# Optimization experiments

Measured on AMD Instinct MI355X. Metric: run time of the kernel, lower is better.

## Reference

```python
import jax, jax.numpy as jnp
import numpy as np

N_NODES = 50000
N_EDGES = 600000
N_GRAPHS = 512
LN_EPS = 1e-5


def setup_inputs() -> dict:
    key = jax.random.key(0)
    ks = jax.random.split(key, 18)
    s = 0.05
    return {
        "x": jax.random.normal(ks[0], (N_NODES, 29), jnp.float32),
        "xdims": jax.random.normal(ks[1], (N_NODES, 3), jnp.float32),
        "xsttype": jax.random.randint(ks[2], (N_NODES,), 0, 256),
        "edge_index": jax.random.randint(ks[3], (2, N_EDGES), 0, N_NODES),
        "batch": jnp.sort(jax.random.randint(ks[4], (N_NODES,), 0, N_GRAPHS)),
        "st_emb": jax.random.normal(ks[5], (256, 12), jnp.float32) * s,
        "Wl1": jax.random.normal(ks[6], (128, 44), jnp.float32) * s,
        "bl1": jnp.zeros((128,), jnp.float32),
        "Wr1": jax.random.normal(ks[7], (128, 44), jnp.float32) * s,
        "g1": jnp.ones((128,), jnp.float32),
        "beta1": jnp.zeros((128,), jnp.float32),
        "Wl2": jax.random.normal(ks[8], (128, 128), jnp.float32) * s,
        "bl2": jnp.zeros((128,), jnp.float32),
        "Wr2": jax.random.normal(ks[9], (128, 128), jnp.float32) * s,
        "g2": jnp.ones((128,), jnp.float32),
        "beta2": jnp.zeros((128,), jnp.float32),
        "Wlin": jax.random.normal(ks[10], (10, 256), jnp.float32) * s,
        "blin": jnp.zeros((10,), jnp.float32),
    }


def layernorm(h, g, b):
    mu = jnp.mean(h, axis=-1, keepdims=True)
    var = jnp.mean(jnp.square(h - mu), axis=-1, keepdims=True)
    return g * (h - mu) * jax.lax.rsqrt(var + LN_EPS) + b


def sage_conv(h, src, dst, Wl, bl, Wr):
    # PyG SAGEConv: lin_l(mean_j x_j) + lin_r(x_i); messages flow src -> dst.
    msg = h[src]                                            # [E, D]
    agg = jax.ops.segment_sum(msg, dst, num_segments=N_NODES)
    cnt = jax.ops.segment_sum(jnp.ones((msg.shape[0],), h.dtype), dst, num_segments=N_NODES)
    mean = agg / jnp.maximum(cnt, 1.0)[:, None]
    return mean @ Wl.T + bl + h @ Wr.T


def reference(x, xdims, xsttype, edge_index, batch, st_emb,
              Wl1, bl1, Wr1, g1, beta1,
              Wl2, bl2, Wr2, g2, beta2,
              Wlin, blin):
    src, dst = edge_index[0], edge_index[1]
    h = jnp.concatenate([x, xdims, st_emb[xsttype]], axis=1)   # [N, 44]
    # Layer 1
    h = jax.nn.relu(layernorm(sage_conv(h, src, dst, Wl1, bl1, Wr1), g1, beta1))
    # Layer 2
    h = jax.nn.relu(layernorm(sage_conv(h, src, dst, Wl2, bl2, Wr2), g2, beta2))
    # dropout inactive (inference)
    hs = jax.ops.segment_sum(h, batch, num_segments=N_GRAPHS)
    nc = jax.ops.segment_sum(jnp.ones((h.shape[0],), h.dtype), batch, num_segments=N_GRAPHS)
    hmean = hs / jnp.maximum(nc, 1.0)[:, None]
    hmax = jax.ops.segment_max(h, batch, num_segments=N_GRAPHS)
    pooled = jnp.concatenate([hmean, hmax], axis=1)            # [G, 256]
    return pooled @ Wlin.T + blin                              # [G, 10]
```

## Files before the change

### kernel.cpp

```cpp
#include <hip/hip_runtime.h>
#include <hip/hip_bf16.h>
#include <math.h>

#define N_NODES 50000
#define N_EDGES 600000
#define N_GRAPHS 512
#define LN_EPS 1e-5f
#define CAP 64
#define NPB 128
#define NBINS ((N_NODES + NPB - 1) / NPB)
#define BCAP 2048
#define BPAD 16
#define PREP_BLOCKS ((N_NODES * 8 + 255) / 256)

typedef short bf16x8 __attribute__((ext_vector_type(8)));
typedef float f32x4 __attribute__((ext_vector_type(4)));

__device__ __forceinline__ unsigned short f2bf(float f) {
    unsigned int x = __float_as_uint(f);
    return (unsigned short)((x + 0x7fffu + ((x >> 16) & 1u)) >> 16);
}
__device__ __forceinline__ float bflo(unsigned int u) { return __uint_as_float(u << 16); }
__device__ __forceinline__ float bfhi(unsigned int u) { return __uint_as_float(u & 0xffff0000u); }

__global__ __launch_bounds__(256) void prep_kernel(
    const float* __restrict__ x, const float* __restrict__ xdims,
    const int* __restrict__ stt, const float* __restrict__ st_emb,
    const float* __restrict__ Wl1, const float* __restrict__ Wr1,
    const float* __restrict__ Wl2, const float* __restrict__ Wr2,
    const int* __restrict__ batch,
    unsigned short* __restrict__ Xh1, unsigned short* __restrict__ Wc1,
    unsigned short* __restrict__ Wc2, int* __restrict__ binCnt,
    int* __restrict__ starts)
{
    int idx = blockIdx.x * 256 + threadIdx.x;

    if (idx < N_NODES * 8) {
        int n = idx >> 3;
        int c0 = (idx & 7) * 8;
        float vv[8];
        #pragma unroll
        for (int j = 0; j < 8; ++j) {
            int c = c0 + j;
            float v;
            if (c < 29)       v = x[n * 29 + c];
            else if (c < 32)  v = xdims[n * 3 + (c - 29)];
            else if (c < 44)  v = st_emb[stt[n] * 12 + (c - 32)];
            else              v = 0.f;
            vv[j] = v;
        }
        uint4 p;
        p.x = (unsigned int)f2bf(vv[0]) | ((unsigned int)f2bf(vv[1]) << 16);
        p.y = (unsigned int)f2bf(vv[2]) | ((unsigned int)f2bf(vv[3]) << 16);
        p.z = (unsigned int)f2bf(vv[4]) | ((unsigned int)f2bf(vv[5]) << 16);
        p.w = (unsigned int)f2bf(vv[6]) | ((unsigned int)f2bf(vv[7]) << 16);
        ((uint4*)Xh1)[idx] = p;
    }
    if (idx < 128 * 128) {
        int f = idx >> 7, k = idx & 127;
        float v;
        if (k < 44)        v = Wr1[f * 44 + k];
        else if (k < 64)   v = 0.f;
        else if (k < 108)  v = Wl1[f * 44 + (k - 64)];
        else               v = 0.f;
        Wc1[idx] = f2bf(v);
    }
    if (idx < 128 * 256) {
        int f = idx >> 8, k = idx & 255;
        float v = (k < 128) ? Wr2[f * 128 + k] : Wl2[f * 128 + (k - 128)];
        Wc2[idx] = f2bf(v);
    }
    if (idx < N_NODES) {
        int b = batch[idx];
        int pb = (idx == 0) ? -1 : batch[idx - 1];
        for (int g = pb + 1; g <= b; ++g) starts[g] = idx;
        if (idx == N_NODES - 1)
            for (int g = b + 1; g <= N_GRAPHS; ++g) starts[g] = N_NODES;
    }
    if (idx < NBINS * BPAD) binCnt[idx] = 0;
}

__global__ __launch_bounds__(1024) void bin_scatter_kernel(
    const int* __restrict__ esrc_in, const int* __restrict__ edst_in,
    int* __restrict__ binCnt, unsigned int* __restrict__ binBuf)
{
    __shared__ int cntL[NBINS];
    __shared__ int gbaseL[NBINS];
    const int tid = threadIdx.x;
    for (int i = tid; i < NBINS; i += 1024) cntL[i] = 0;
    __syncthreads();

    int e4 = (blockIdx.x * 1024 + tid) * 4;
    int4 d4, s4; int b0=0,b1=0,b2=0,b3=0, r0=0,r1=0,r2=0,r3=0;
    const bool valid = e4 < N_EDGES;
    if (valid) {
        d4 = *(const int4*)(edst_in + e4);
        s4 = *(const int4*)(esrc_in + e4);
        b0 = d4.x >> 7; b1 = d4.y >> 7; b2 = d4.z >> 7; b3 = d4.w >> 7;
        r0 = atomicAdd(&cntL[b0], 1);
        r1 = atomicAdd(&cntL[b1], 1);
        r2 = atomicAdd(&cntL[b2], 1);
        r3 = atomicAdd(&cntL[b3], 1);
    }
    __syncthreads();
    for (int i = tid; i < NBINS; i += 1024) {
        int c = cntL[i];
        gbaseL[i] = (c > 0) ? atomicAdd(&binCnt[i * BPAD], c) : 0;
    }
    __syncthreads();
    if (valid) {
        int p0 = gbaseL[b0] + r0, p1 = gbaseL[b1] + r1;
        int p2 = gbaseL[b2] + r2, p3 = gbaseL[b3] + r3;
        if (p0 < BCAP) binBuf[(size_t)b0 * BCAP + p0] = (((unsigned)d4.x & 127u) << 16) | (unsigned)s4.x;
        if (p1 < BCAP) binBuf[(size_t)b1 * BCAP + p1] = (((unsigned)d4.y & 127u) << 16) | (unsigned)s4.y;
        if (p2 < BCAP) binBuf[(size_t)b2 * BCAP + p2] = (((unsigned)d4.z & 127u) << 16) | (unsigned)s4.z;
        if (p3 < BCAP) binBuf[(size_t)b3 * BCAP + p3] = (((unsigned)d4.w & 127u) << 16) | (unsigned)s4.w;
    }
}

__global__ __launch_bounds__(256) void bin_adj_kernel(
    const int* __restrict__ binCnt, const unsigned int* __restrict__ binBuf,
    unsigned short* __restrict__ adj, int* __restrict__ cnt)
{
    __shared__ int cl[NPB];
    const int b = blockIdx.x;
    const int tid = threadIdx.x;
    if (tid < NPB) cl[tid] = 0;
    __syncthreads();
    int ec = binCnt[b * BPAD]; if (ec > BCAP) ec = BCAP;
    const unsigned int* buf = binBuf + (size_t)b * BCAP;
    for (int i = tid; i < ec; i += 256) {
        unsigned int p = buf[i];
        int dl = (int)(p >> 16);
        int slot = atomicAdd(&cl[dl], 1);
        if (slot < CAP)
            adj[((size_t)(b * NPB + dl)) * CAP + slot] = (unsigned short)(p & 0xFFFFu);
    }
    __syncthreads();
    if (tid < NPB) {
        int n = b * NPB + tid;
        if (n < N_NODES) cnt[n] = cl[tid];
    }
}

template <int DHALF, int NPW>
__global__ __launch_bounds__(256) void agg_kernel(const int* __restrict__ cnt,
                                                  const unsigned short* __restrict__ adj,
                                                  const unsigned short* __restrict__ Xh,
                                                  unsigned short* __restrict__ M)
{
    constexpr int CH  = DHALF / 8;
    constexpr int LPN = 64 / NPW;
    constexpr int NG  = LPN / CH;
    constexpr int NL  = 16 / NG;
    const int lane = threadIdx.x & 63;
    const int wv   = threadIdx.x >> 6;
    const int ln   = lane % LPN;
    const int nbl  = lane - ln;
    const int grp  = ln / CH;
    const int sl   = ln % CH;
    const int n = (blockIdx.x * 4 + wv) * NPW + (lane / LPN);

    int degT = cnt[n];
    int deg  = (degT < CAP) ? degT : CAP;
    unsigned int er32 = ((const unsigned int*)adj)[(size_t)n * (CAP / 2) + ln];
    float a0=0.f,a1=0.f,a2=0.f,a3=0.f,a4=0.f,a5=0.f,a6=0.f,a7=0.f;
    const uint4* gbase = (const uint4*)Xh;
    const int c1 = deg - 1;
    const int lim1 = (2 * LPN >= CAP) ? deg : ((deg < 2 * LPN) ? deg : 2 * LPN);
    for (int e = 0; e < lim1; e += 16) {
        uint4 v[NL]; float mk[NL];
        #pragma unroll
        for (int j = 0; j < NL; ++j) {
            int ee = e + j * NG + grp;
            int eec = (ee < c1) ? ee : c1;
            unsigned int u = __shfl(er32, nbl + (eec >> 1));
            int s = (eec & 1) ? (int)(u >> 16) : (int)(u & 0xFFFFu);
            v[j]  = gbase[(size_t)s * CH + sl];
            mk[j] = (ee < deg) ? 1.f : 0.f;
        }
        #pragma unroll
        for (int j = 0; j < NL; ++j) {
            a0 += mk[j] * bflo(v[j].x); a1 += mk[j] * bfhi(v[j].x);
            a2 += mk[j] * bflo(v[j].y); a3 += mk[j] * bfhi(v[j].y);
            a4 += mk[j] * bflo(v[j].z); a5 += mk[j] * bfhi(v[j].z);
            a6 += mk[j] * bflo(v[j].w); a7 += mk[j] * bfhi(v[j].w);
        }
    }
    if (2 * LPN < CAP) {
        for (int e = 2 * LPN; e < deg; e += 16) {
            uint4 v[NL]; float mk[NL];
            #pragma unroll
            for (int j = 0; j < NL; ++j) {
                int ee = e + j * NG + grp;
                int eec = (ee < c1) ? ee : c1;
                int s = (int)adj[(size_t)n * CAP + eec];
                v[j]  = gbase[(size_t)s * CH + sl];
                mk[j] = (ee < deg) ? 1.f : 0.f;
            }
            #pragma unroll
            for (int j = 0; j < NL; ++j) {
                a0 += mk[j] * bflo(v[j].x); a1 += mk[j] * bfhi(v[j].x);
                a2 += mk[j] * bflo(v[j].y); a3 += mk[j] * bfhi(v[j].y);
                a4 += mk[j] * bflo(v[j].z); a5 += mk[j] * bfhi(v[j].z);
                a6 += mk[j] * bflo(v[j].w); a7 += mk[j] * bfhi(v[j].w);
            }
        }
    }
    a0 += __shfl_xor(a0, CH); a1 += __shfl_xor(a1, CH);
    a2 += __shfl_xor(a2, CH); a3 += __shfl_xor(a3, CH);
    a4 += __shfl_xor(a4, CH); a5 += __shfl_xor(a5, CH);
    a6 += __shfl_xor(a6, CH); a7 += __shfl_xor(a7, CH);

    if (grp == 0) {
        float inv = (degT > 0) ? 1.f / (float)degT : 0.f;
        uint4 p;
        p.x = (unsigned int)f2bf(a0 * inv) | ((unsigned int)f2bf(a1 * inv) << 16);
        p.y = (unsigned int)f2bf(a2 * inv) | ((unsigned int)f2bf(a3 * inv) << 16);
        p.z = (unsigned int)f2bf(a4 * inv) | ((unsigned int)f2bf(a5 * inv) << 16);
        p.w = (unsigned int)f2bf(a6 * inv) | ((unsigned int)f2bf(a7 * inv) << 16);
        ((uint4*)M)[(size_t)n * CH + sl] = p;
    }
}

template <int KPAD>
__global__ __launch_bounds__(256) void mfma_layer_kernel(
    const unsigned short* __restrict__ Xh, const unsigned short* __restrict__ M,
    const unsigned short* __restrict__ W,
    const float* __restrict__ bl, const float* __restrict__ g,
    const float* __restrict__ beta,
    unsigned short* __restrict__ Out)
{
    constexpr int DHALF = KPAD / 2;
    const int lane = threadIdx.x & 63;
    const int wv   = threadIdx.x >> 6;
    const int l15  = lane & 15;
    const int l4   = lane >> 4;
    const int row0 = blockIdx.x * 128 + wv * 32;

    int rA0 = row0 + l15;       if (rA0 > N_NODES - 1) rA0 = N_NODES - 1;
    int rA1 = row0 + 16 + l15;  if (rA1 > N_NODES - 1) rA1 = N_NODES - 1;

    f32x4 acc[2][8];
    #pragma unroll
    for (int m = 0; m < 2; ++m)
        #pragma unroll
        for (int n = 0; n < 8; ++n) acc[m][n] = (f32x4){0.f, 0.f, 0.f, 0.f};

    const int kb = l4 * 8;
    #pragma unroll
    for (int ks = 0; ks < KPAD / 32; ++ks) {
        const int k = ks * 32 + kb;
        bf16x8 a0, a1;
        if (ks < DHALF / 32) {
            a0 = *(const bf16x8*)(Xh + (size_t)rA0 * DHALF + k);
            a1 = *(const bf16x8*)(Xh + (size_t)rA1 * DHALF + k);
        } else {
            a0 = *(const bf16x8*)(M + (size_t)rA0 * DHALF + (k - DHALF));
            a1 = *(const bf16x8*)(M + (size_t)rA1 * DHALF + (k - DHALF));
        }
        #pragma unroll
        for (int ni = 0; ni < 8; ++ni) {
            bf16x8 b = *(const bf16x8*)(W + (size_t)(ni * 16 + l15) * KPAD + k);
            acc[0][ni] = __builtin_amdgcn_mfma_f32_16x16x32_bf16(a0, b, acc[0][ni], 0, 0, 0);
            acc[1][ni] = __builtin_amdgcn_mfma_f32_16x16x32_bf16(a1, b, acc[1][ni], 0, 0, 0);
        }
    }

    float blv[8], gv[8], bev[8];
    #pragma unroll
    for (int ni = 0; ni < 8; ++ni) {
        int f = ni * 16 + l15;
        blv[ni] = bl[f]; gv[ni] = g[f]; bev[ni] = beta[f];
    }

    #pragma unroll
    for (int mi = 0; mi < 2; ++mi) {
        #pragma unroll
        for (int r = 0; r < 4; ++r) {
            float v[8];
            float s1 = 0.f, s2 = 0.f;
            #pragma unroll
            for (int ni = 0; ni < 8; ++ni) {
                float t = acc[mi][ni][r] + blv[ni];
                v[ni] = t; s1 += t; s2 += t * t;
            }
            #pragma unroll
            for (int m = 8; m >= 1; m >>= 1) {
                s1 += __shfl_xor(s1, m);
                s2 += __shfl_xor(s2, m);
            }
            float mu   = s1 * (1.f / 128.f);
            float var  = s2 * (1.f / 128.f) - mu * mu;
            float rstd = rsqrtf(var + LN_EPS);
            int node = row0 + mi * 16 + l4 * 4 + r;
            if (node < N_NODES) {
                #pragma unroll
                for (int ni = 0; ni < 8; ++ni) {
                    float o = gv[ni] * (v[ni] - mu) * rstd + bev[ni];
                    o = fmaxf(o, 0.f);
                    Out[(size_t)node * 128 + ni * 16 + l15] = f2bf(o);
                }
            }
        }
    }
}

__global__ __launch_bounds__(256) void poolhead_kernel(const unsigned short* __restrict__ h2,
                                                       const int* __restrict__ starts,
                                                       const float* __restrict__ Wlin,
                                                       const float* __restrict__ blin,
                                                       float* __restrict__ out)
{
    const int g  = blockIdx.x;
    const int j2 = threadIdx.x & 63;
    const int h  = threadIdx.x >> 6;
    const int s0 = starts[g], s1 = starts[g + 1];
    float sa = 0.f, sb = 0.f, ma = -INFINITY, mb = -INFINITY;
    const unsigned int* base = (const unsigned int*)h2;
    int n = s0 + h;
    for (; n + 4 < s1; n += 8) {
        unsigned int u0 = base[(size_t)n * 64 + j2];
        unsigned int u1 = base[(size_t)(n + 4) * 64 + j2];
        float l0 = bflo(u0), h0 = bfhi(u0);
        float l1 = bflo(u1), h1 = bfhi(u1);
        sa += l0 + l1; sb += h0 + h1;
        ma = fmaxf(ma, fmaxf(l0, l1));
        mb = fmaxf(mb, fmaxf(h0, h1));
    }
    if (n < s1) {
        unsigned int u = base[(size_t)n * 64 + j2];
        float lo = bflo(u), hi = bfhi(u);
        sa += lo; sb += hi;
        ma = fmaxf(ma, lo); mb = fmaxf(mb, hi);
    }
    __shared__ float red[4][4][64];
    __shared__ float pooled[256];
    red[h][0][j2] = sa; red[h][1][j2] = sb; red[h][2][j2] = ma; red[h][3][j2] = mb;
    __syncthreads();
    if (h == 0) {
        #pragma unroll
        for (int o = 1; o < 4; ++o) {
            sa += red[o][0][j2]; sb += red[o][1][j2];
            ma = fmaxf(ma, red[o][2][j2]); mb = fmaxf(mb, red[o][3][j2]);
        }
        int c = s1 - s0;
        float inv = (c > 0) ? 1.f / (float)c : 0.f;
        pooled[2 * j2]           = sa * inv;
        pooled[2 * j2 + 1]       = sb * inv;
        pooled[128 + 2 * j2]     = (c > 0) ? ma : 0.f;
        pooled[128 + 2 * j2 + 1] = (c > 0) ? mb : 0.f;
    }
    __syncthreads();
    if (threadIdx.x < 10) {
        const float* w = Wlin + threadIdx.x * 256;
        float acc = blin[threadIdx.x];
        for (int k = 0; k < 256; ++k) acc += pooled[k] * w[k];
        out[g * 10 + threadIdx.x] = acc;
    }
}

extern "C" void kernel_launch(void* const* d_in, const int* in_sizes, int n_in,
                              void* d_out, int out_size, void* d_ws, size_t ws_size,
                              hipStream_t stream)
{
    const float* x      = (const float*)d_in[0];
    const float* xdims  = (const float*)d_in[1];
    const int*   stt    = (const int*)d_in[2];
    const int*   eidx   = (const int*)d_in[3];
    const int*   batch  = (const int*)d_in[4];
    const float* st_emb = (const float*)d_in[5];
    const float* Wl1 = (const float*)d_in[6];
    const float* bl1 = (const float*)d_in[7];
    const float* Wr1 = (const float*)d_in[8];
    const float* g1  = (const float*)d_in[9];
    const float* be1 = (const float*)d_in[10];
    const float* Wl2 = (const float*)d_in[11];
    const float* bl2 = (const float*)d_in[12];
    const float* Wr2 = (const float*)d_in[13];
    const float* g2  = (const float*)d_in[14];
    const float* be2 = (const float*)d_in[15];
    const float* Wlin = (const float*)d_in[16];
    const float* blin = (const float*)d_in[17];
    float* out = (float*)d_out;

    const int* esrc_in = eidx;
    const int* edst_in = eidx + N_EDGES;

    char* ws = (char*)d_ws;
    size_t o = 0;
    auto carve = [&](size_t bytes) { void* p = ws + o; o = (o + bytes + 255) & ~(size_t)255; return p; };
    unsigned short* Xh1  = (unsigned short*)carve((size_t)N_NODES * 64 * 2);
    unsigned short* M1   = (unsigned short*)carve((size_t)N_NODES * 64 * 2);
    unsigned short* Xh2  = (unsigned short*)carve((size_t)N_NODES * 128 * 2);
    unsigned short* M2   = (unsigned short*)carve((size_t)N_NODES * 128 * 2);
    unsigned short* h2bf = (unsigned short*)carve((size_t)N_NODES * 128 * 2);
    unsigned short* Wc1  = (unsigned short*)carve((size_t)128 * 128 * 2);
    unsigned short* Wc2  = (unsigned short*)carve((size_t)128 * 256 * 2);
    int*            cnt  = (int*)carve((size_t)N_NODES * 4);
    int*          binCnt = (int*)carve((size_t)NBINS * BPAD * 4);
    unsigned int* binBuf = (unsigned int*)carve((size_t)NBINS * BCAP * 4);
    unsigned short* adj  = (unsigned short*)carve((size_t)(NBINS * NPB) * CAP * 2);
    int*          starts = (int*)carve((size_t)(N_GRAPHS + 1) * 4);
    (void)ws_size;

    prep_kernel<<<PREP_BLOCKS, 256, 0, stream>>>(
        x, xdims, stt, st_emb, Wl1, Wr1, Wl2, Wr2, batch,
        Xh1, Wc1, Wc2, binCnt, starts);

    bin_scatter_kernel<<<(N_EDGES / 4 + 1023) / 1024, 1024, 0, stream>>>(
        esrc_in, edst_in, binCnt, binBuf);

    bin_adj_kernel<<<NBINS, 256, 0, stream>>>(binCnt, binBuf, adj, cnt);

    agg_kernel<64, 4><<<N_NODES / 16, 256, 0, stream>>>(cnt, adj, Xh1, M1);
    mfma_layer_kernel<128><<<(N_NODES + 127) / 128, 256, 0, stream>>>(
        Xh1, M1, Wc1, bl1, g1, be1, Xh2);

    agg_kernel<128, 2><<<N_NODES / 8, 256, 0, stream>>>(cnt, adj, Xh2, M2);
    mfma_layer_kernel<256><<<(N_NODES + 127) / 128, 256, 0, stream>>>(
        Xh2, M2, Wc2, bl2, g2, be2, h2bf);

    poolhead_kernel<<<N_GRAPHS, 256, 0, stream>>>(h2bf, starts, Wlin, blin, out);
}
```

Baseline: 112.5 us.

## Locally sort edges by bin in shared memory before coalesced scatter to bins

The bin scatter kernel now counts edges per bin in shared memory, takes an exclusive prefix scan of those counts, and places each edge into a block-local sorted buffer. It then writes to the global bin buffers in sorted order, so neighbouring threads write contiguous addresses and the scattered global writes become coalesced. The packed word now carries the full dst index, so bin_adj masks it to get the local node. Separately, the layer-2 aggregation switches to 4 nodes per wave with one lane group, which skips the cross-group shuffle. The costs are a 512-step-log scan with many barriers and about 20KB more LDS per block.

```diff
diff --git a/kernel.cpp b/kernel.cpp
--- a/kernel.cpp
+++ b/kernel.cpp
@@ -12,6 +12,8 @@
 #define BCAP 2048
 #define BPAD 16
 #define PREP_BLOCKS ((N_NODES * 8 + 255) / 256)
+#define P1_EPB 4096
+#define P1_BLOCKS ((N_EDGES + P1_EPB - 1) / P1_EPB)
 
 typedef short bf16x8 __attribute__((ext_vector_type(8)));
 typedef float f32x4 __attribute__((ext_vector_type(4)));
@@ -85,36 +87,64 @@
     int* __restrict__ binCnt, unsigned int* __restrict__ binBuf)
 {
     __shared__ int cntL[NBINS];
+    __shared__ int startL[NBINS];
     __shared__ int gbaseL[NBINS];
+    __shared__ int s[512];
+    __shared__ unsigned int sortedL[P1_EPB];
     const int tid = threadIdx.x;
+    const int e0 = blockIdx.x * P1_EPB;
+    const int tcount = (N_EDGES - e0 < P1_EPB) ? (N_EDGES - e0) : P1_EPB;
+
     for (int i = tid; i < NBINS; i += 1024) cntL[i] = 0;
     __syncthreads();
 
-    int e4 = (blockIdx.x * 1024 + tid) * 4;
-    int4 d4, s4; int b0=0,b1=0,b2=0,b3=0, r0=0,r1=0,r2=0,r3=0;
+    int e4 = e0 + tid * 4;
     const bool valid = e4 < N_EDGES;
+    unsigned int pk[4]; int bb[4], rk[4];
     if (valid) {
-        d4 = *(const int4*)(edst_in + e4);
-        s4 = *(const int4*)(esrc_in + e4);
-        b0 = d4.x >> 7; b1 = d4.y >> 7; b2 = d4.z >> 7; b3 = d4.w >> 7;
-        r0 = atomicAdd(&cntL[b0], 1);
-        r1 = atomicAdd(&cntL[b1], 1);
-        r2 = atomicAdd(&cntL[b2], 1);
-        r3 = atomicAdd(&cntL[b3], 1);
-    }
-    __syncthreads();
-    for (int i = tid; i < NBINS; i += 1024) {
-        int c = cntL[i];
-        gbaseL[i] = (c > 0) ? atomicAdd(&binCnt[i * BPAD], c) : 0;
-    }
-    __syncthreads();
+        int4 d4 = *(const int4*)(edst_in + e4);
+        int4 s4 = *(const int4*)(esrc_in + e4);
+        pk[0] = ((unsigned)d4.x << 16) | (unsigned)s4.x;
+        pk[1] = ((unsigned)d4.y << 16) | (unsigned)s4.y;
+        pk[2] = ((unsigned)d4.z << 16) | (unsigned)s4.z;
+        pk[3] = ((unsigned)d4.w << 16) | (unsigned)s4.w;
+        bb[0] = d4.x >> 7; bb[1] = d4.y >> 7; bb[2] = d4.z >> 7; bb[3] = d4.w >> 7;
+        rk[0] = atomicAdd(&cntL[bb[0]], 1);
+        rk[1] = atomicAdd(&cntL[bb[1]], 1);
+        rk[2] = atomicAdd(&cntL[bb[2]], 1);
+        rk[3] = atomicAdd(&cntL[bb[3]], 1);
+    }
+    __syncthreads();
+
+    if (tid < 512) s[tid] = (tid < NBINS) ? cntL[tid] : 0;
+    __syncthreads();
+    for (int d = 1; d < 512; d <<= 1) {
+        int t = 0;
+        if (tid < 512 && tid >= d) t = s[tid - d];
+        __syncthreads();
+        if (tid < 512) s[tid] += t;
+        __syncthreads();
+    }
+    if (tid < NBINS) {
+        startL[tid] = s[tid] - cntL[tid];
+        int c = cntL[tid];
+        gbaseL[tid] = (c > 0) ? atomicAdd(&binCnt[tid * BPAD], c) : 0;
+    }
+    __syncthreads();
+
     if (valid) {
-        int p0 = gbaseL[b0] + r0, p1 = gbaseL[b1] + r1;
-        int p2 = gbaseL[b2] + r2, p3 = gbaseL[b3] + r3;
-        if (p0 < BCAP) binBuf[(size_t)b0 * BCAP + p0] = (((unsigned)d4.x & 127u) << 16) | (unsigned)s4.x;
-        if (p1 < BCAP) binBuf[(size_t)b1 * BCAP + p1] = (((unsigned)d4.y & 127u) << 16) | (unsigned)s4.y;
-        if (p2 < BCAP) binBuf[(size_t)b2 * BCAP + p2] = (((unsigned)d4.z & 127u) << 16) | (unsigned)s4.z;
-        if (p3 < BCAP) binBuf[(size_t)b3 * BCAP + p3] = (((unsigned)d4.w & 127u) << 16) | (unsigned)s4.w;
+        sortedL[startL[bb[0]] + rk[0]] = pk[0];
+        sortedL[startL[bb[1]] + rk[1]] = pk[1];
+        sortedL[startL[bb[2]] + rk[2]] = pk[2];
+        sortedL[startL[bb[3]] + rk[3]] = pk[3];
+    }
+    __syncthreads();
+
+    for (int i = tid; i < tcount; i += 1024) {
+        unsigned int v = sortedL[i];
+        int b = (int)(v >> 23);
+        int off = gbaseL[b] + (i - startL[b]);
+        if (off < BCAP) binBuf[(size_t)b * BCAP + off] = v;
     }
 }
 
@@ -131,7 +161,7 @@
     const unsigned int* buf = binBuf + (size_t)b * BCAP;
     for (int i = tid; i < ec; i += 256) {
         unsigned int p = buf[i];
-        int dl = (int)(p >> 16);
+        int dl = (int)((p >> 16) & 127u);
         int slot = atomicAdd(&cl[dl], 1);
         if (slot < CAP)
             adj[((size_t)(b * NPB + dl)) * CAP + slot] = (unsigned short)(p & 0xFFFFu);
@@ -207,10 +237,12 @@
             }
         }
     }
-    a0 += __shfl_xor(a0, CH); a1 += __shfl_xor(a1, CH);
-    a2 += __shfl_xor(a2, CH); a3 += __shfl_xor(a3, CH);
-    a4 += __shfl_xor(a4, CH); a5 += __shfl_xor(a5, CH);
-    a6 += __shfl_xor(a6, CH); a7 += __shfl_xor(a7, CH);
+    if (NG > 1) {
+        a0 += __shfl_xor(a0, CH); a1 += __shfl_xor(a1, CH);
+        a2 += __shfl_xor(a2, CH); a3 += __shfl_xor(a3, CH);
+        a4 += __shfl_xor(a4, CH); a5 += __shfl_xor(a5, CH);
+        a6 += __shfl_xor(a6, CH); a7 += __shfl_xor(a7, CH);
+    }
 
     if (grp == 0) {
         float inv = (degT > 0) ? 1.f / (float)degT : 0.f;
@@ -408,7 +440,7 @@
         x, xdims, stt, st_emb, Wl1, Wr1, Wl2, Wr2, batch,
         Xh1, Wc1, Wc2, binCnt, starts);
 
-    bin_scatter_kernel<<<(N_EDGES / 4 + 1023) / 1024, 1024, 0, stream>>>(
+    bin_scatter_kernel<<<P1_BLOCKS, 1024, 0, stream>>>(
         esrc_in, edst_in, binCnt, binBuf);
 
     bin_adj_kernel<<<NBINS, 256, 0, stream>>>(binCnt, binBuf, adj, cnt);
@@ -417,7 +449,7 @@
     mfma_layer_kernel<128><<<(N_NODES + 127) / 128, 256, 0, stream>>>(
         Xh1, M1, Wc1, bl1, g1, be1, Xh2);
 
-    agg_kernel<128, 2><<<N_NODES / 8, 256, 0, stream>>>(cnt, adj, Xh2, M2);
+    agg_kernel<128, 4><<<N_NODES / 16, 256, 0, stream>>>(cnt, adj, Xh2, M2);
     mfma_layer_kernel<256><<<(N_NODES + 127) / 128, 256, 0, stream>>>(
         Xh2, M2, Wc2, bl2, g2, be2, h2bf);
 
```

Result: slower. 118.9 us (+5.7%).
